# Kernel optimization log

Hardware: AMD Instinct MI355X
Metric: run time of the kernel (lower is better)

The kernel has to match this reference:

```python
import jax, jax.numpy as jnp
import numpy as np

EPS = 1e-5
TOP_K = 50

def _layernorm(h, g, b):
    mu = jnp.mean(h, axis=-1, keepdims=True)
    var = jnp.mean((h - mu) ** 2, axis=-1, keepdims=True)
    return (h - mu) * jax.lax.rsqrt(var + EPS) * g + b

def setup_inputs() -> dict:
    key = jax.random.key(0)
    ks = jax.random.split(key, 8)
    B, D, E = 16384, 384, 2048
    return {
        "x": jax.random.normal(ks[0], (B, D), jnp.float32),
        "We": jax.random.normal(ks[1], (D, E), jnp.float32) * 0.05,
        "be": jax.random.normal(ks[2], (E,), jnp.float32) * 0.01,
        "g1": jnp.ones((E,), jnp.float32),
        "b1": jnp.zeros((E,), jnp.float32),
        "Wd": jax.random.normal(ks[3], (E, D), jnp.float32) * 0.02,
        "bd": jax.random.normal(ks[4], (D,), jnp.float32) * 0.01,
        "Wb": jax.random.normal(ks[5], (E, D), jnp.float32) * 0.02,
        "bb": jax.random.normal(ks[6], (D,), jnp.float32) * 0.01,
        "g2": jnp.ones((D,), jnp.float32),
        "b2": jnp.zeros((D,), jnp.float32),
    }

def reference(x, We, be, g1, b1, Wd, bd, Wb, bb, g2, b2):
    # encoder: Linear -> LayerNorm -> ReLU
    h = jax.nn.relu(_layernorm(x @ We + be, g1, b1))  # [B, E]
    # top-k sparsification: zero all but top-50 per row (scatter mask, matches torch)
    _, idx = jax.lax.top_k(h, TOP_K)                  # [B, K]
    rows = jnp.arange(h.shape[0])[:, None]
    mask = jnp.zeros_like(h).at[rows, idx].set(1.0)
    sparse = h * mask                                 # [B, E]
    recon = sparse @ Wd + bd                          # [B, D]
    separated = _layernorm(sparse @ Wb + bb, g2, b2)  # [B, D]
    return recon, sparse, separated
```

## Files before the change

### kernel.cpp

```cpp
#include <hip/hip_runtime.h>
#include <hip/hip_bf16.h>
#include <stdint.h>

#define B_D   384
#define B_E   2048
#define TOPK  50
#define LN_EPS 1e-5f
#define NKS   18
#define NKP   12
#define FIX_WINDOW 2e-4f

typedef short bf16x8 __attribute__((ext_vector_type(8)));
typedef float f32x4  __attribute__((ext_vector_type(4)));

__device__ __forceinline__ float wave_sum_f(float v) {
#pragma unroll
    for (int d = 1; d < 64; d <<= 1) v += __shfl_xor(v, d, 64);
    return v;
}
__device__ __forceinline__ int wave_sum_i(int v) {
#pragma unroll
    for (int d = 1; d < 64; d <<= 1) v += __shfl_xor(v, d, 64);
    return v;
}
__device__ __forceinline__ float wave_max_f(float v) {
#pragma unroll
    for (int d = 1; d < 64; d <<= 1) v = fmaxf(v, __shfl_xor(v, d, 64));
    return v;
}

__device__ __forceinline__ ushort f2bf_hi(float v) {
    __hip_bfloat16 b = __float2bfloat16(v);
    return *(ushort*)&b;
}
__device__ __forceinline__ ushort f2bf_lo(float v) {
    __hip_bfloat16 b = __float2bfloat16(v);
    float rem = v - __bfloat162float(b);
    __hip_bfloat16 l = __float2bfloat16(rem);
    return *(ushort*)&l;
}

__device__ __forceinline__ void llds16(const void* g, void* l) {
    __builtin_amdgcn_global_load_lds((const __attribute__((address_space(1))) void*)g,
                                     (__attribute__((address_space(3))) void*)l, 16, 0, 0);
}

__global__ __launch_bounds__(256) void pack_A(const float* __restrict__ x, ushort* __restrict__ Ap,
                                              int* __restrict__ cntr)
{
    const int ks = blockIdx.x, mt = blockIdx.y, t = threadIdx.x;
    if (cntr && t == 0 && ks == 0 && mt == 0) *cntr = 0;
#pragma unroll
    for (int q = 0; q < 4; ++q) {
        const int s = q * 256 + t;
        const int m = s & 127, kg = s >> 7;
        const int kp = ks * 64 + kg * 8;
        const int hi = (kp < 384);
        const int ksrc = hi ? kp : kp - 384;
        const float* src = x + (size_t)(mt * 128 + m) * B_D + ksrc;
        float4 v0 = *(const float4*)src;
        float4 v1 = *(const float4*)(src + 4);
        float vv[8] = {v0.x, v0.y, v0.z, v0.w, v1.x, v1.y, v1.z, v1.w};
        ushort o[8];
#pragma unroll
        for (int e = 0; e < 8; ++e)
            o[e] = hi ? f2bf_hi(vv[e]) : f2bf_lo(vv[e]);
        *(uint4*)(Ap + ((size_t)(mt * NKP + ks) * 1024 + s) * 8) = *(uint4*)o;
    }
}

__global__ __launch_bounds__(256) void pack_B(const float* __restrict__ We, ushort* __restrict__ Bp)
{
    const int ks = blockIdx.x, nt = blockIdx.y, t = threadIdx.x;
#pragma unroll
    for (int q = 0; q < 4; ++q) {
        const int s = q * 256 + t;
        const int nl = s & 127, kg = s >> 7;
        const int kp = ks * 64 + kg * 8;
        const int hi = (kp < 384);
        const int ksrc = hi ? kp : kp - 384;
        const int ng = nt * 128 + nl;
        ushort o[8];
#pragma unroll
        for (int e = 0; e < 8; ++e) {
            float v = We[(size_t)(ksrc + e) * B_E + ng];
            o[e] = hi ? f2bf_hi(v) : f2bf_lo(v);
        }
        *(uint4*)(Bp + ((size_t)(nt * NKP + ks) * 1024 + s) * 8) = *(uint4*)o;
    }
}

__global__ __launch_bounds__(128) void pack_W(
    const float* __restrict__ Wd, const float* __restrict__ Wb, uint* __restrict__ Wp)
{
    const int e = blockIdx.x, t = threadIdx.x;
#pragma unroll
    for (int j = 0; j < 3; ++j) {
        const int c = t + 128 * j;
        const ushort d = f2bf_hi(Wd[(size_t)e * B_D + c]);
        const ushort b = f2bf_hi(Wb[(size_t)e * B_D + c]);
        Wp[(size_t)e * B_D + c] = ((uint)b << 16) | (uint)d;
    }
}

__global__ __launch_bounds__(256) void enc_mfma(
    const ushort* __restrict__ Ap, const ushort* __restrict__ Bp,
    const float* __restrict__ be, float* __restrict__ y)
{
    __shared__ __align__(16) ushort As[8192];
    __shared__ __align__(16) ushort Bs[8192];
    const int t = threadIdx.x, lane = t & 63, w = t >> 6;
    const int wr = w >> 1, wc = w & 1;
    const int mt = blockIdx.y, nt = blockIdx.x;
    const ushort* gA = Ap + (size_t)mt * NKP * 8192;
    const ushort* gB = Bp + (size_t)nt * NKP * 8192;

    f32x4 acc[4][4];
#pragma unroll
    for (int i = 0; i < 4; ++i)
#pragma unroll
        for (int j = 0; j < 4; ++j)
#pragma unroll
            for (int r = 0; r < 4; ++r) acc[i][j][r] = 0.f;

    const int l15 = lane & 15, l4 = lane >> 4;
    for (int ls = 0; ls < NKS; ++ls) {
        const int ksA = (ls < 6) ? ls : ls - 6;
        const int ksB = (ls < 12) ? ls : ls - 12;
        const ushort* a_src = gA + (size_t)ksA * 8192 + t * 8;
        const ushort* b_src = gB + (size_t)ksB * 8192 + t * 8;
#pragma unroll
        for (int q = 0; q < 4; ++q) {
            llds16(a_src + q * 2048, &As[t * 8 + q * 2048]);
            llds16(b_src + q * 2048, &Bs[t * 8 + q * 2048]);
        }
        __syncthreads();
#pragma unroll
        for (int ko = 0; ko < 2; ++ko) {
            const int kg = ko * 4 + l4;
            bf16x8 af[4], bfr[4];
#pragma unroll
            for (int i = 0; i < 4; ++i)
                af[i] = *(const bf16x8*)&As[(kg * 128 + wr * 64 + i * 16 + l15) * 8];
#pragma unroll
            for (int j = 0; j < 4; ++j)
                bfr[j] = *(const bf16x8*)&Bs[(kg * 128 + wc * 64 + j * 16 + l15) * 8];
#pragma unroll
            for (int i = 0; i < 4; ++i)
#pragma unroll
                for (int j = 0; j < 4; ++j)
                    acc[i][j] = __builtin_amdgcn_mfma_f32_16x16x32_bf16(af[i], bfr[j], acc[i][j], 0, 0, 0);
        }
        __syncthreads();
    }
    float bev[4];
#pragma unroll
    for (int j = 0; j < 4; ++j) bev[j] = be[nt * 128 + wc * 64 + j * 16 + l15];
#pragma unroll
    for (int i = 0; i < 4; ++i)
#pragma unroll
        for (int j = 0; j < 4; ++j)
#pragma unroll
            for (int r = 0; r < 4; ++r) {
                const int row = mt * 128 + wr * 64 + i * 16 + l4 * 4 + r;
                const int col = nt * 128 + wc * 64 + j * 16 + l15;
                y[(size_t)row * B_E + col] = acc[i][j][r] + bev[j];
            }
}

__global__ __launch_bounds__(256) void enc_gemm_f32(
    const float* __restrict__ x, const float* __restrict__ We,
    const float* __restrict__ be, float* __restrict__ y)
{
    __shared__ float As[8][128];
    __shared__ float Bs[8][128];
    const int t  = threadIdx.x;
    const int m0 = blockIdx.y * 128;
    const int n0 = blockIdx.x * 128;
    const int tx = t & 15, ty = t >> 4;
    const int la_m = t >> 1, la_k = (t & 1) * 4;
    const int lb_k = t >> 5, lb_c = (t & 31) * 4;

    float acc[8][8];
#pragma unroll
    for (int i = 0; i < 8; ++i)
#pragma unroll
        for (int j = 0; j < 8; ++j) acc[i][j] = 0.f;

    for (int k0 = 0; k0 < B_D; k0 += 8) {
        float4 a = *(const float4*)&x[(size_t)(m0 + la_m) * B_D + k0 + la_k];
        float4 b = *(const float4*)&We[(size_t)(k0 + lb_k) * B_E + n0 + lb_c];
        __syncthreads();
        As[la_k + 0][la_m] = a.x;
        As[la_k + 1][la_m] = a.y;
        As[la_k + 2][la_m] = a.z;
        As[la_k + 3][la_m] = a.w;
        *(float4*)&Bs[lb_k][lb_c] = b;
        __syncthreads();
#pragma unroll
        for (int kk = 0; kk < 8; ++kk) {
            float4 a0 = *(const float4*)&As[kk][ty * 4];
            float4 a1 = *(const float4*)&As[kk][ty * 4 + 64];
            float4 b0 = *(const float4*)&Bs[kk][tx * 4];
            float4 b1 = *(const float4*)&Bs[kk][tx * 4 + 64];
            float av[8] = {a0.x,a0.y,a0.z,a0.w,a1.x,a1.y,a1.z,a1.w};
            float bv[8] = {b0.x,b0.y,b0.z,b0.w,b1.x,b1.y,b1.z,b1.w};
#pragma unroll
            for (int i = 0; i < 8; ++i)
#pragma unroll
                for (int j = 0; j < 8; ++j)
                    acc[i][j] = fmaf(av[i], bv[j], acc[i][j]);
        }
    }
    float4 beL = *(const float4*)&be[n0 + tx * 4];
    float4 beH = *(const float4*)&be[n0 + 64 + tx * 4];
    float bl[8] = {beL.x,beL.y,beL.z,beL.w,beH.x,beH.y,beH.z,beH.w};
#pragma unroll
    for (int i = 0; i < 8; ++i) {
        int row = m0 + ty * 4 + (i & 3) + (i >> 2) * 64;
        float4 o0 = {acc[i][0]+bl[0], acc[i][1]+bl[1], acc[i][2]+bl[2], acc[i][3]+bl[3]};
        float4 o1 = {acc[i][4]+bl[4], acc[i][5]+bl[5], acc[i][6]+bl[6], acc[i][7]+bl[7]};
        *(float4*)&y[(size_t)row * B_E + n0 + tx * 4]      = o0;
        *(float4*)&y[(size_t)row * B_E + n0 + 64 + tx * 4] = o1;
    }
}

__device__ __forceinline__ int ln_topk_row(
    float (&h)[32], int lane, const float* __restrict__ g1, const float* __restrict__ b1,
    float* __restrict__ row, int* __restrict__ IwR, float* __restrict__ VwR,
    float* __restrict__ ldsv, int* __restrict__ ldsi)
{
    float s = 0.f;
#pragma unroll
    for (int j = 0; j < 32; ++j) s += h[j];
    s = wave_sum_f(s);
    const float mu = s * (1.f / B_E);
    float ss = 0.f;
#pragma unroll
    for (int j = 0; j < 32; ++j) { float d = h[j] - mu; ss += d * d; }
    ss = wave_sum_f(ss);
    const float rstd = rsqrtf(ss * (1.f / B_E) + LN_EPS);
#pragma unroll
    for (int q = 0; q < 8; ++q) {
        float4 g  = *(const float4*)&g1[q * 256 + lane * 4];
        float4 bb = *(const float4*)&b1[q * 256 + lane * 4];
        float gg[4]  = {g.x,g.y,g.z,g.w};
        float bbv[4] = {bb.x,bb.y,bb.z,bb.w};
#pragma unroll
        for (int i = 0; i < 4; ++i) {
            int j = q*4+i;
            h[j] = fmaxf(fmaf((h[j] - mu) * rstd, gg[i], bbv[i]), 0.f);
        }
    }
    float mx = h[0];
#pragma unroll
    for (int j = 1; j < 32; ++j) mx = fmaxf(mx, h[j]);
    mx = wave_max_f(mx);

    float vlo = 0.f, vhi = __uint_as_float(__float_as_uint(mx) + 1u);
    int cl = 2048;
    bool window = false;
    for (int it = 0; it < 20; ++it) {
        float mid = 0.5f * (vlo + vhi);
        if (it == 0 && 2.2f > vlo && 2.2f < vhi) mid = 2.2f;
        if (!(mid > vlo && mid < vhi)) break;
        int c = 0;
#pragma unroll
        for (int j = 0; j < 32; ++j)
            c += (int)__popcll(__ballot(h[j] >= mid));
        if (c >= TOPK) { vlo = mid; cl = c; if (c <= 64) { window = true; break; } }
        else vhi = mid;
    }
    unsigned lo = __float_as_uint(vlo);
    if (!window) {
        unsigned hi = __float_as_uint(vhi);
        while (hi - lo > 1u) {
            const unsigned mid = lo + ((hi - lo) >> 1);
            const float mf = __uint_as_float(mid);
            int c = 0;
#pragma unroll
            for (int j = 0; j < 32; ++j)
                c += (int)__popcll(__ballot(h[j] >= mf));
            if (c >= TOPK) { lo = mid; cl = c; if (c <= 64) break; }
            else hi = mid;
        }
    }
    const float T0 = __uint_as_float(lo);

    unsigned selmask = 0u;
    int flag = 0;
    bool fastSel = (cl <= 64 && T0 > 0.f);

    if (fastSel) {
        ldsv[lane] = -1.f;
        ldsi[lane] = 1 << 20;
        asm volatile("s_waitcnt lgkmcnt(0)" ::: "memory");
        int base = 0;
#pragma unroll
        for (int j = 0; j < 32; ++j) {
            const bool p = (h[j] >= T0);
            const unsigned long long m = __ballot(p);
            if (p) {
                const int pos = base + (int)__popcll(m & ((1ull << lane) - 1ull));
                ldsv[pos] = h[j];
                ldsi[pos] = (j >> 2) * 256 + lane * 4 + (j & 3);
            }
            base += (int)__popcll(m);
        }
        asm volatile("s_waitcnt lgkmcnt(0)" ::: "memory");
        float sv = ldsv[lane];
        int   si = ldsi[lane];
#pragma unroll
        for (int k = 2; k <= 64; k <<= 1) {
#pragma unroll
            for (int jj = k >> 1; jj > 0; jj >>= 1) {
                const float ov = __shfl_xor(sv, jj, 64);
                const int   oi = __shfl_xor(si, jj, 64);
                const bool dirUp = ((lane & k) == 0);
                const bool lower = ((lane & jj) == 0);
                const bool mineBefore = (sv > ov) || (sv == ov && si < oi);
                const bool keep = (lower == dirUp) ? mineBefore : !mineBefore;
                if (!keep) { sv = ov; si = oi; }
            }
        }
        const float T    = __shfl(sv, TOPK - 1, 64);
        const int   idxT = __shfl(si, TOPK - 1, 64);
        float v51;
        if (cl > TOPK) {
            v51 = __shfl(sv, TOPK, 64);
        } else {
            float bb = -1.f;
#pragma unroll
            for (int j = 0; j < 32; ++j) bb = (h[j] < T0) ? fmaxf(bb, h[j]) : bb;
            v51 = wave_max_f(bb);
        }
        flag = (T - v51 < FIX_WINDOW) ? 1 : 0;
#pragma unroll
        for (int j = 0; j < 32; ++j) {
            const int e = (j >> 2) * 256 + lane * 4 + (j & 3);
            if (h[j] > T || (h[j] == T && e <= idxT)) selmask |= (1u << j);
        }
        if (lane < TOPK) { IwR[lane] = si; VwR[lane] = sv; }
    } else {
        const float T = T0;
        int cgt = 0, ceq = 0;
        float below = -1.f;
#pragma unroll
        for (int j = 0; j < 32; ++j) {
            cgt += (h[j] > T); ceq += (h[j] == T);
            if (h[j] < T) below = fmaxf(below, h[j]);
        }
        const int cgt_t = wave_sum_i(cgt);
        const int ceq_t = wave_sum_i(ceq);
        below = wave_max_f(below);
        const int need = TOPK - cgt_t;

        if (cgt_t + ceq_t == TOPK) {
#pragma unroll
            for (int j = 0; j < 32; ++j) if (h[j] >= T) selmask |= (1u << j);
        } else {
            int base = 0;
            for (int q = 0; q < 8; ++q) {
                int tc = 0;
#pragma unroll
                for (int i = 0; i < 4; ++i) tc += (h[q*4+i] == T);
                int ip = tc;
#pragma unroll
                for (int d = 1; d < 64; d <<= 1) {
                    int o = __shfl_up(ip, d, 64);
                    if (lane >= d) ip += o;
                }
                int rk  = base + ip - tc;
                int tot = __shfl(ip, 63, 64);
#pragma unroll
                for (int i = 0; i < 4; ++i) {
                    int j = q*4+i;
                    if (h[j] > T) selmask |= (1u << j);
                    else if (h[j] == T) { if (rk < need) selmask |= (1u << j); rk++; }
                }
                base += tot;
            }
        }
        if (T > 0.f) {
            if (cgt_t + ceq_t != TOPK && ceq_t > need) flag = 1;
            else if (T - below < FIX_WINDOW) flag = 1;
        }
        const int myc = __popc(selmask);
        int ip = myc;
#pragma unroll
        for (int d = 1; d < 64; d <<= 1) {
            int o = __shfl_up(ip, d, 64);
            if (lane >= d) ip += o;
        }
        int pos = ip - myc;
        for (int j = 0; j < 32; ++j) {
            if ((selmask >> j) & 1u) {
                int e = (j >> 2) * 256 + lane * 4 + (j & 3);
                IwR[pos] = e;
                VwR[pos] = h[j];
                pos++;
            }
        }
    }

#pragma unroll
    for (int q = 0; q < 8; ++q) {
        float4 o;
        o.x = ((selmask >> (q*4+0)) & 1u) ? h[q*4+0] : 0.f;
        o.y = ((selmask >> (q*4+1)) & 1u) ? h[q*4+1] : 0.f;
        o.z = ((selmask >> (q*4+2)) & 1u) ? h[q*4+2] : 0.f;
        o.w = ((selmask >> (q*4+3)) & 1u) ? h[q*4+3] : 0.f;
        *(float4*)&row[q * 256 + lane * 4] = o;
    }
    return flag;
}

__global__ __launch_bounds__(256) void ln_relu_topk_k(
    float* __restrict__ y, const float* __restrict__ g1, const float* __restrict__ b1,
    int* __restrict__ Iw, float* __restrict__ Vw,
    int* __restrict__ flags, int* __restrict__ rowlist, int* __restrict__ cntr)
{
    __shared__ float ldsv[4][64];
    __shared__ int   ldsi[4][64];
    const int lane = threadIdx.x & 63;
    const int w = threadIdx.x >> 6;
    const int r = blockIdx.x * 4 + w;
    float* row = y + (size_t)r * B_E;
    float h[32];
#pragma unroll
    for (int q = 0; q < 8; ++q) {
        float4 v = *(const float4*)&row[q * 256 + lane * 4];
        h[q*4+0] = v.x; h[q*4+1] = v.y; h[q*4+2] = v.z; h[q*4+3] = v.w;
    }
    int flag = ln_topk_row(h, lane, g1, b1, row, Iw + r * TOPK, Vw + r * TOPK,
                           ldsv[w], ldsi[w]);
    if (flags && lane == 0) {
        flags[r] = flag;
        if (flag) {
            int p = atomicAdd(cntr, 1);
            rowlist[p] = r;
        }
    }
}

__global__ __launch_bounds__(256) void fixup_recompute(
    const float* __restrict__ x, const float* __restrict__ We, const float* __restrict__ be,
    float* __restrict__ y, const int* __restrict__ rowlist, const int* __restrict__ cntr)
{
    const int nflag = *cntr;
    const int rb = blockIdx.y * 8;
    if (rb >= nflag) return;
    const int nact = min(nflag - rb, 8);
    const int t = threadIdx.x;

    __shared__ float xs[8][B_D];
    __shared__ int   rIdx[8];
    if (t < 8) rIdx[t] = (t < nact) ? rowlist[rb + t] : -1;
    __syncthreads();
#pragma unroll
    for (int i = 0; i < 8; ++i) {
        if (i < nact) {
            const float* src = x + (size_t)rIdx[i] * B_D;
            for (int j = t; j < B_D; j += 256) xs[i][j] = src[j];
        } else {
            for (int j = t; j < B_D; j += 256) xs[i][j] = 0.f;
        }
    }
    __syncthreads();

    const int c = blockIdx.x * 256 + t;
    const float bc = be[c];
    float acc[8];
#pragma unroll
    for (int i = 0; i < 8; ++i) acc[i] = bc;
#pragma unroll 4
    for (int k = 0; k < B_D; ++k) {
        const float w = We[(size_t)k * B_E + c];
#pragma unroll
        for (int i = 0; i < 8; ++i) acc[i] = fmaf(xs[i][k], w, acc[i]);
    }
#pragma unroll
    for (int i = 0; i < 8; ++i)
        if (i < nact) y[(size_t)rIdx[i] * B_E + c] = acc[i];
}

__global__ __launch_bounds__(256) void fixup_select(
    float* __restrict__ y, const float* __restrict__ g1, const float* __restrict__ b1,
    int* __restrict__ Iw, float* __restrict__ Vw, const int* __restrict__ flags)
{
    __shared__ float ldsv[4][64];
    __shared__ int   ldsi[4][64];
    const int w = threadIdx.x >> 6;
    const int r = blockIdx.x * 4 + w;
    if (!flags[r]) return;
    const int lane = threadIdx.x & 63;
    float* row = y + (size_t)r * B_E;
    float h[32];
#pragma unroll
    for (int q = 0; q < 8; ++q) {
        float4 v = *(const float4*)&row[q * 256 + lane * 4];
        h[q*4+0] = v.x; h[q*4+1] = v.y; h[q*4+2] = v.z; h[q*4+3] = v.w;
    }
    ln_topk_row(h, lane, g1, b1, row, Iw + r * TOPK, Vw + r * TOPK,
                ldsv[w], ldsi[w]);
}

__global__ __launch_bounds__(128) void decode_packed(
    const int* __restrict__ Iw, const float* __restrict__ Vw,
    const uint* __restrict__ Wp, const float* __restrict__ bd,
    const float* __restrict__ bbias, const float* __restrict__ g2,
    const float* __restrict__ b2, float* __restrict__ recon, float* __restrict__ sep)
{
    __shared__ int   sI[TOPK];
    __shared__ float sV[TOPK];
    __shared__ float red[2];
    const int r = blockIdx.x, t = threadIdx.x;
    if (t < TOPK) { sI[t] = Iw[r * TOPK + t]; sV[t] = Vw[r * TOPK + t]; }
    __syncthreads();
    float ad[3], ab[3];
#pragma unroll
    for (int j = 0; j < 3; ++j) { ad[j] = bd[t + 128*j]; ab[j] = bbias[t + 128*j]; }
#pragma unroll 2
    for (int i = 0; i < TOPK; ++i) {
        const int   idx = sI[i];
        const float v   = sV[i];
        const uint* wp  = Wp + (size_t)idx * B_D;
#pragma unroll
        for (int j = 0; j < 3; ++j) {
            const uint u = wp[t + 128*j];
            const float wd = __uint_as_float(u << 16);
            const float wb = __uint_as_float(u & 0xFFFF0000u);
            ad[j] = fmaf(v, wd, ad[j]);
            ab[j] = fmaf(v, wb, ab[j]);
        }
    }
#pragma unroll
    for (int j = 0; j < 3; ++j) recon[(size_t)r * B_D + t + 128*j] = ad[j];
    float s = ab[0] + ab[1] + ab[2];
    s = wave_sum_f(s);
    if ((t & 63) == 0) red[t >> 6] = s;
    __syncthreads();
    const float mu = (red[0] + red[1]) * (1.f / B_D);
    __syncthreads();
    float ss = 0.f;
#pragma unroll
    for (int j = 0; j < 3; ++j) { float d = ab[j] - mu; ss += d * d; }
    ss = wave_sum_f(ss);
    if ((t & 63) == 0) red[t >> 6] = ss;
    __syncthreads();
    const float rstd = rsqrtf((red[0] + red[1]) * (1.f / B_D) + LN_EPS);
#pragma unroll
    for (int j = 0; j < 3; ++j) {
        int c = t + 128*j;
        sep[(size_t)r * B_D + c] = fmaf((ab[j] - mu) * rstd, g2[c], b2[c]);
    }
}

__global__ __launch_bounds__(128) void decode_f32(
    const int* __restrict__ Iw, const float* __restrict__ Vw,
    const float* __restrict__ Wd, const float* __restrict__ bd,
    const float* __restrict__ Wb, const float* __restrict__ bbias,
    const float* __restrict__ g2, const float* __restrict__ b2,
    float* __restrict__ recon, float* __restrict__ sep)
{
    __shared__ int   sI[TOPK];
    __shared__ float sV[TOPK];
    __shared__ float red[2];
    const int r = blockIdx.x, t = threadIdx.x;
    if (t < TOPK) { sI[t] = Iw[r * TOPK + t]; sV[t] = Vw[r * TOPK + t]; }
    __syncthreads();
    float ad[3], ab[3];
#pragma unroll
    for (int j = 0; j < 3; ++j) { ad[j] = bd[t + 128*j]; ab[j] = bbias[t + 128*j]; }
#pragma unroll 2
    for (int i = 0; i < TOPK; ++i) {
        const int   idx = sI[i];
        const float v   = sV[i];
        const float* wd = Wd + (size_t)idx * B_D;
        const float* wb = Wb + (size_t)idx * B_D;
#pragma unroll
        for (int j = 0; j < 3; ++j) {
            ad[j] = fmaf(v, wd[t + 128*j], ad[j]);
            ab[j] = fmaf(v, wb[t + 128*j], ab[j]);
        }
    }
#pragma unroll
    for (int j = 0; j < 3; ++j) recon[(size_t)r * B_D + t + 128*j] = ad[j];
    float s = ab[0] + ab[1] + ab[2];
    s = wave_sum_f(s);
    if ((t & 63) == 0) red[t >> 6] = s;
    __syncthreads();
    const float mu = (red[0] + red[1]) * (1.f / B_D);
    __syncthreads();
    float ss = 0.f;
#pragma unroll
    for (int j = 0; j < 3; ++j) { float d = ab[j] - mu; ss += d * d; }
    ss = wave_sum_f(ss);
    if ((t & 63) == 0) red[t >> 6] = ss;
    __syncthreads();
    const float rstd = rsqrtf((red[0] + red[1]) * (1.f / B_D) + LN_EPS);
#pragma unroll
    for (int j = 0; j < 3; ++j) {
        int c = t + 128*j;
        sep[(size_t)r * B_D + c] = fmaf((ab[j] - mu) * rstd, g2[c], b2[c]);
    }
}

extern "C" void kernel_launch(void* const* d_in, const int* in_sizes, int n_in,
                              void* d_out, int out_size, void* d_ws, size_t ws_size,
                              hipStream_t stream)
{
    const float* x  = (const float*)d_in[0];
    const float* We = (const float*)d_in[1];
    const float* be = (const float*)d_in[2];
    const float* g1 = (const float*)d_in[3];
    const float* b1 = (const float*)d_in[4];
    const float* Wd = (const float*)d_in[5];
    const float* bd = (const float*)d_in[6];
    const float* Wb = (const float*)d_in[7];
    const float* bb = (const float*)d_in[8];
    const float* g2 = (const float*)d_in[9];
    const float* b2 = (const float*)d_in[10];

    const int Brows = in_sizes[0] / B_D;
    float* recon  = (float*)d_out;
    float* sparse = recon + (size_t)Brows * B_D;
    float* sep    = sparse + (size_t)Brows * B_E;

    char* ws = (char*)d_ws;
    int*   Iw      = (int*)ws;
    float* Vw      = (float*)(ws + 3276800);
    int*   flags   = (int*)(ws + 6553600);
    int*   rowlist = (int*)(ws + 6619136);
    int*   cntr    = (int*)(ws + 6684672);
    const size_t apOff = 6688768;
    const size_t bpOff = apOff + (size_t)128 * NKP * 1024 * 16;
    const size_t need  = bpOff + (size_t)16 * NKP * 1024 * 16;

    if (ws_size >= need) {
        ushort* Ap = (ushort*)(ws + apOff);
        ushort* Bp = (ushort*)(ws + bpOff);
        uint*   Wp = (uint*)(ws + apOff);
        pack_A<<<dim3(NKP, 128), dim3(256), 0, stream>>>(x, Ap, cntr);
        pack_B<<<dim3(NKP, 16),  dim3(256), 0, stream>>>(We, Bp);
        enc_mfma<<<dim3(16, 128), dim3(256), 0, stream>>>(Ap, Bp, be, sparse);
        pack_W<<<dim3(B_E), dim3(128), 0, stream>>>(Wd, Wb, Wp);
        ln_relu_topk_k<<<dim3(Brows / 4), dim3(256), 0, stream>>>(sparse, g1, b1, Iw, Vw, flags, rowlist, cntr);
        fixup_recompute<<<dim3(8, Brows / 8), dim3(256), 0, stream>>>(x, We, be, sparse, rowlist, cntr);
        fixup_select<<<dim3(Brows / 4), dim3(256), 0, stream>>>(sparse, g1, b1, Iw, Vw, flags);
        decode_packed<<<dim3(Brows), dim3(128), 0, stream>>>(Iw, Vw, Wp, bd, bb, g2, b2, recon, sep);
    } else {
        enc_gemm_f32<<<dim3(16, 128), dim3(256), 0, stream>>>(x, We, be, sparse);
        ln_relu_topk_k<<<dim3(Brows / 4), dim3(256), 0, stream>>>(sparse, g1, b1, Iw, Vw, nullptr, nullptr, nullptr);
        decode_f32<<<dim3(Brows), dim3(128), 0, stream>>>(Iw, Vw, Wd, bd, Wb, bb, g2, b2, recon, sep);
    }
}
```

Before: 291.3 us.

## Enlarge encoder MFMA tile to 256x256 with double-buffered LDS and swizzled grid

Changes the encoder GEMM from 128x128 tiles with 4 waves to 256x256 tiles with 8 waves, each wave now computing 128x64. Packing kernels are rewritten for the larger tile layout. LDS is double buffered so the next k-slice loads while MFMAs run, which removes one barrier per step, and the block index is swizzled to improve L2 reuse. The aim is more data reuse per loaded byte and overlap of loads with compute. The cost is 128KB of LDS and 128 accumulator registers per thread, so occupancy drops.

```diff
diff --git a/kernel.cpp b/kernel.cpp
--- a/kernel.cpp
+++ b/kernel.cpp
@@ -51,13 +51,13 @@
     const int ks = blockIdx.x, mt = blockIdx.y, t = threadIdx.x;
     if (cntr && t == 0 && ks == 0 && mt == 0) *cntr = 0;
 #pragma unroll
-    for (int q = 0; q < 4; ++q) {
+    for (int q = 0; q < 8; ++q) {
         const int s = q * 256 + t;
-        const int m = s & 127, kg = s >> 7;
+        const int m = s & 255, kg = s >> 8;
         const int kp = ks * 64 + kg * 8;
         const int hi = (kp < 384);
         const int ksrc = hi ? kp : kp - 384;
-        const float* src = x + (size_t)(mt * 128 + m) * B_D + ksrc;
+        const float* src = x + (size_t)(mt * 256 + m) * B_D + ksrc;
         float4 v0 = *(const float4*)src;
         float4 v1 = *(const float4*)(src + 4);
         float vv[8] = {v0.x, v0.y, v0.z, v0.w, v1.x, v1.y, v1.z, v1.w};
@@ -65,7 +65,7 @@
 #pragma unroll
         for (int e = 0; e < 8; ++e)
             o[e] = hi ? f2bf_hi(vv[e]) : f2bf_lo(vv[e]);
-        *(uint4*)(Ap + ((size_t)(mt * NKP + ks) * 1024 + s) * 8) = *(uint4*)o;
+        *(uint4*)(Ap + ((size_t)(mt * NKP + ks) * 2048 + s) * 8) = *(uint4*)o;
     }
 }
 
@@ -73,20 +73,20 @@
 {
     const int ks = blockIdx.x, nt = blockIdx.y, t = threadIdx.x;
 #pragma unroll
-    for (int q = 0; q < 4; ++q) {
+    for (int q = 0; q < 8; ++q) {
         const int s = q * 256 + t;
-        const int nl = s & 127, kg = s >> 7;
+        const int nl = s & 255, kg = s >> 8;
         const int kp = ks * 64 + kg * 8;
         const int hi = (kp < 384);
         const int ksrc = hi ? kp : kp - 384;
-        const int ng = nt * 128 + nl;
+        const int ng = nt * 256 + nl;
         ushort o[8];
 #pragma unroll
         for (int e = 0; e < 8; ++e) {
             float v = We[(size_t)(ksrc + e) * B_E + ng];
             o[e] = hi ? f2bf_hi(v) : f2bf_lo(v);
         }
-        *(uint4*)(Bp + ((size_t)(nt * NKP + ks) * 1024 + s) * 8) = *(uint4*)o;
+        *(uint4*)(Bp + ((size_t)(nt * NKP + ks) * 2048 + s) * 8) = *(uint4*)o;
     }
 }
 
@@ -103,67 +103,81 @@
     }
 }
 
-__global__ __launch_bounds__(256) void enc_mfma(
+__global__ __launch_bounds__(512, 2) void enc_mfma256(
     const ushort* __restrict__ Ap, const ushort* __restrict__ Bp,
     const float* __restrict__ be, float* __restrict__ y)
 {
-    __shared__ __align__(16) ushort As[8192];
-    __shared__ __align__(16) ushort Bs[8192];
+    __shared__ __align__(16) ushort As[2][16384];
+    __shared__ __align__(16) ushort Bs[2][16384];
     const int t = threadIdx.x, lane = t & 63, w = t >> 6;
-    const int wr = w >> 1, wc = w & 1;
-    const int mt = blockIdx.y, nt = blockIdx.x;
-    const ushort* gA = Ap + (size_t)mt * NKP * 8192;
-    const ushort* gB = Bp + (size_t)nt * NKP * 8192;
-
-    f32x4 acc[4][4];
-#pragma unroll
-    for (int i = 0; i < 4; ++i)
+    const int wr = w >> 2, wc = w & 3;
+    const int gid = blockIdx.x;
+    const int swz = (gid & 7) * 64 + (gid >> 3);
+    const int nt = swz & 7, mt = swz >> 3;
+    const ushort* gA = Ap + (size_t)mt * NKP * 16384;
+    const ushort* gB = Bp + (size_t)nt * NKP * 16384;
+
+    f32x4 acc[8][4];
+#pragma unroll
+    for (int i = 0; i < 8; ++i)
 #pragma unroll
         for (int j = 0; j < 4; ++j)
 #pragma unroll
             for (int r = 0; r < 4; ++r) acc[i][j][r] = 0.f;
 
     const int l15 = lane & 15, l4 = lane >> 4;
+
+#define STAGE256(ls_, buf_)                                                     \
+    {                                                                           \
+        const int lsv = (ls_);                                                  \
+        const int ksA = (lsv < 6) ? lsv : lsv - 6;                              \
+        const int ksB = (lsv < 12) ? lsv : lsv - 12;                            \
+        const ushort* a_src = gA + (size_t)ksA * 16384 + t * 8;                 \
+        const ushort* b_src = gB + (size_t)ksB * 16384 + t * 8;                 \
+        _Pragma("unroll")                                                       \
+        for (int q = 0; q < 4; ++q) {                                           \
+            llds16(a_src + q * 4096, &As[buf_][t * 8 + q * 4096]);              \
+            llds16(b_src + q * 4096, &Bs[buf_][t * 8 + q * 4096]);              \
+        }                                                                       \
+    }
+
+    STAGE256(0, 0);
+    __syncthreads();
+
     for (int ls = 0; ls < NKS; ++ls) {
-        const int ksA = (ls < 6) ? ls : ls - 6;
-        const int ksB = (ls < 12) ? ls : ls - 12;
-        const ushort* a_src = gA + (size_t)ksA * 8192 + t * 8;
-        const ushort* b_src = gB + (size_t)ksB * 8192 + t * 8;
-#pragma unroll
-        for (int q = 0; q < 4; ++q) {
-            llds16(a_src + q * 2048, &As[t * 8 + q * 2048]);
-            llds16(b_src + q * 2048, &Bs[t * 8 + q * 2048]);
-        }
-        __syncthreads();
+        const int cur = ls & 1;
+        if (ls + 1 < NKS) STAGE256(ls + 1, cur ^ 1);
 #pragma unroll
         for (int ko = 0; ko < 2; ++ko) {
             const int kg = ko * 4 + l4;
-            bf16x8 af[4], bfr[4];
-#pragma unroll
-            for (int i = 0; i < 4; ++i)
-                af[i] = *(const bf16x8*)&As[(kg * 128 + wr * 64 + i * 16 + l15) * 8];
+            bf16x8 af[8], bfr[4];
+#pragma unroll
+            for (int i = 0; i < 8; ++i)
+                af[i] = *(const bf16x8*)&As[cur][(kg * 256 + wr * 128 + i * 16 + l15) * 8];
 #pragma unroll
             for (int j = 0; j < 4; ++j)
-                bfr[j] = *(const bf16x8*)&Bs[(kg * 128 + wc * 64 + j * 16 + l15) * 8];
-#pragma unroll
-            for (int i = 0; i < 4; ++i)
+                bfr[j] = *(const bf16x8*)&Bs[cur][(kg * 256 + wc * 64 + j * 16 + l15) * 8];
+#pragma unroll
+            for (int i = 0; i < 8; ++i)
 #pragma unroll
                 for (int j = 0; j < 4; ++j)
                     acc[i][j] = __builtin_amdgcn_mfma_f32_16x16x32_bf16(af[i], bfr[j], acc[i][j], 0, 0, 0);
         }
-        __syncthreads();
-    }
+        if (ls + 1 < NKS) __syncthreads();
+    }
+#undef STAGE256
+
     float bev[4];
 #pragma unroll
-    for (int j = 0; j < 4; ++j) bev[j] = be[nt * 128 + wc * 64 + j * 16 + l15];
-#pragma unroll
-    for (int i = 0; i < 4; ++i)
+    for (int j = 0; j < 4; ++j) bev[j] = be[nt * 256 + wc * 64 + j * 16 + l15];
+#pragma unroll
+    for (int i = 0; i < 8; ++i)
 #pragma unroll
         for (int j = 0; j < 4; ++j)
 #pragma unroll
             for (int r = 0; r < 4; ++r) {
-                const int row = mt * 128 + wr * 64 + i * 16 + l4 * 4 + r;
-                const int col = nt * 128 + wc * 64 + j * 16 + l15;
+                const int row = mt * 256 + wr * 128 + i * 16 + l4 * 4 + r;
+                const int col = nt * 256 + wc * 64 + j * 16 + l15;
                 y[(size_t)row * B_E + col] = acc[i][j][r] + bev[j];
             }
 }
@@ -634,16 +648,16 @@
     int*   rowlist = (int*)(ws + 6619136);
     int*   cntr    = (int*)(ws + 6684672);
     const size_t apOff = 6688768;
-    const size_t bpOff = apOff + (size_t)128 * NKP * 1024 * 16;
-    const size_t need  = bpOff + (size_t)16 * NKP * 1024 * 16;
+    const size_t bpOff = apOff + (size_t)64 * NKP * 2048 * 16;
+    const size_t need  = bpOff + (size_t)8 * NKP * 2048 * 16;
 
     if (ws_size >= need) {
         ushort* Ap = (ushort*)(ws + apOff);
         ushort* Bp = (ushort*)(ws + bpOff);
         uint*   Wp = (uint*)(ws + apOff);
-        pack_A<<<dim3(NKP, 128), dim3(256), 0, stream>>>(x, Ap, cntr);
-        pack_B<<<dim3(NKP, 16),  dim3(256), 0, stream>>>(We, Bp);
-        enc_mfma<<<dim3(16, 128), dim3(256), 0, stream>>>(Ap, Bp, be, sparse);
+        pack_A<<<dim3(NKP, 64), dim3(256), 0, stream>>>(x, Ap, cntr);
+        pack_B<<<dim3(NKP, 8),  dim3(256), 0, stream>>>(We, Bp);
+        enc_mfma256<<<dim3(512), dim3(512), 0, stream>>>(Ap, Bp, be, sparse);
         pack_W<<<dim3(B_E), dim3(128), 0, stream>>>(Wd, Wb, Wp);
         ln_relu_topk_k<<<dim3(Brows / 4), dim3(256), 0, stream>>>(sparse, g1, b1, Iw, Vw, flags, rowlist, cntr);
         fixup_recompute<<<dim3(8, Brows / 8), dim3(256), 0, stream>>>(x, We, be, sparse, rowlist, cntr);
```

After: 287.7 us. About the same (-1.2%).
